# Kernel optimization log

Hardware: AMD Instinct MI355X
Metric: run time of the kernel (lower is better)

The kernel has to match this reference:

```python
import jax, jax.numpy as jnp
import numpy as np

V, F_IN, H, DH, T = 512, 8, 64, 4, 3
E, P, L = 8192, 64, 8
D = H + DH  # path-decoder GRU width


def setup_inputs() -> dict:
    key = jax.random.key(0)
    ks = jax.random.split(key, 24)
    s = 0.1
    inp = {
        "adj_matrix": jax.random.normal(ks[0], (V, V, F_IN), jnp.float32),
        "edges": jax.random.randint(ks[1], (E, 2), 0, V),
        "paths": jax.random.randint(ks[2], (P, L), 0, V),
        "demands": jax.random.uniform(ks[3], (P,), jnp.float32),
        "emb_w": jax.random.normal(ks[4], (H, F_IN), jnp.float32) * s,
        "w1s": jax.random.normal(ks[5], (T, H, H), jnp.float32) * s,
        "w2s": jax.random.normal(ks[6], (T, H, H), jnp.float32) * s,
        "w3s": jax.random.normal(ks[7], (T, H, H), jnp.float32) * s,
        "gru_w_ih": jax.random.normal(ks[8], (3 * H, 2 * H), jnp.float32) * s,
        "gru_w_hh": jax.random.normal(ks[9], (3 * H, H), jnp.float32) * s,
        "gru_b_ih": jax.random.normal(ks[10], (3 * H,), jnp.float32) * s,
        "gru_b_hh": jax.random.normal(ks[11], (3 * H,), jnp.float32) * s,
        "pf_w_ih": jax.random.normal(ks[12], (3 * D, D), jnp.float32) * s,
        "pf_w_hh": jax.random.normal(ks[13], (3 * D, D), jnp.float32) * s,
        "pf_b_ih": jax.random.normal(ks[14], (3 * D,), jnp.float32) * s,
        "pf_b_hh": jax.random.normal(ks[15], (3 * D,), jnp.float32) * s,
        "pb_w_ih": jax.random.normal(ks[16], (3 * D, D), jnp.float32) * s,
        "pb_w_hh": jax.random.normal(ks[17], (3 * D, D), jnp.float32) * s,
        "pb_b_ih": jax.random.normal(ks[18], (3 * D,), jnp.float32) * s,
        "pb_b_hh": jax.random.normal(ks[19], (3 * D,), jnp.float32) * s,
        "wq": jax.random.normal(ks[20], (1, D), jnp.float32) * s,
        "bq": jax.random.normal(ks[21], (1,), jnp.float32) * s,
        "wd": jax.random.normal(ks[22], (DH, 1), jnp.float32) * s,
    }
    return inp


def _gru(x_seq, h0, w_ih, w_hh, b_ih, b_hh):
    """torch-style GRU, batch_first. x_seq (B,Tn,I), h0 (B,Hd) -> (ys, h_last)."""
    def step(h, x_t):
        gi = x_t @ w_ih.T + b_ih
        gh = h @ w_hh.T + b_hh
        ir, iz, inn = jnp.split(gi, 3, axis=-1)
        hr, hz, hn = jnp.split(gh, 3, axis=-1)
        r = jax.nn.sigmoid(ir + hr)
        z = jax.nn.sigmoid(iz + hz)
        n = jnp.tanh(inn + r * hn)
        h_new = (1.0 - z) * n + z * h
        return h_new, h_new
    h_last, ys = jax.lax.scan(step, h0, jnp.swapaxes(x_seq, 0, 1))
    return jnp.swapaxes(ys, 0, 1), h_last


def _message_passing(x, u, v, w1, w2, w3):
    """Vectorized form of the per-edge python loop. x (V,V,Hd), u/v (E,)."""
    Hd = x.shape[-1]
    col_sum = x.sum(axis=0)                      # (V,Hd): sum over first index
    nz_row = jnp.sum(x != 0, axis=-1)            # (V,V) nonzero count per entry
    col_nz = nz_row.sum(axis=0)                  # (V,)
    # incoming edges for edge (u,v): column u, row v zeroed, mean over nonzeros
    s_in = col_sum[u] - x[v, u]                  # (E,Hd)
    n_in = (col_nz[u] - nz_row[v, u]).astype(x.dtype) / Hd
    n_in = jnp.where(n_in == 0, 1.0, n_in)
    e_in = s_in / n_in[:, None]
    # outgoing edges: reversed edge (v,u) -> column v, row u zeroed
    s_out = col_sum[v] - x[u, v]
    n_out = (col_nz[v] - nz_row[u, v]).astype(x.dtype) / Hd
    n_out = jnp.where(n_out == 0, 1.0, n_out)
    e_out = s_out / n_out[:, None]
    m = jax.nn.relu(x[u, v] @ w1.T + e_in @ w2.T + e_out @ w3.T)
    return x.at[u, v].set(m)


def reference(adj_matrix, edges, paths, demands, emb_w, w1s, w2s, w3s,
              gru_w_ih, gru_w_hh, gru_b_ih, gru_b_hh,
              pf_w_ih, pf_w_hh, pf_b_ih, pf_b_hh,
              pb_w_ih, pb_w_hh, pb_b_ih, pb_b_hh, wq, bq, wd):
    u, v = edges[:, 0], edges[:, 1]
    x = adj_matrix @ emb_w.T                     # (V,V,H)
    for t in range(T):
        m = _message_passing(x, u, v, w1s[t], w2s[t], w3s[t])
        inp = jnp.concatenate([m, x], axis=-1)   # (V,V,2H)
        x, _ = _gru(inp, jnp.zeros((x.shape[0], H), x.dtype),
                    gru_w_ih, gru_w_hh, gru_b_ih, gru_b_hh)
    demand_emb = jax.nn.relu(demands[:, None] @ wd.T)        # (P,DH)
    graph_emb = jnp.concatenate([x.mean(axis=(0, 1)),
                                 jnp.zeros((DH,), x.dtype)])  # (D,)
    src, dst = paths[:, :-1], paths[:, 1:]                    # (P,L-1)
    edge_feat = x[src, dst]                                   # (P,L-1,H)
    dem = jnp.broadcast_to(demand_emb[:, None, :], (P, L - 1, DH))
    feat = jnp.concatenate([edge_feat, dem], axis=-1)         # (P,L-1,D)
    h0 = jnp.broadcast_to(graph_emb, (P, D))
    _, hf = _gru(feat, h0, pf_w_ih, pf_w_hh, pf_b_ih, pf_b_hh)
    _, hb = _gru(feat[:, ::-1], h0, pb_w_ih, pb_w_hh, pb_b_ih, pb_b_hh)
    paths_emb = (hf + hb) * 0.5                               # mean over directions
    return jax.nn.softmax(paths_emb @ wq.T + bq, axis=0)      # (P,1)
```

## Files before the change

### kernel.cpp

```cpp
#include <hip/hip_runtime.h>


__device__ __forceinline__ float fsig_(float x) { return 1.f / (1.f + __expf(-x)); }
__device__ __forceinline__ float ftanh_(float x) {
  float e = __expf(2.f * x);
  return 1.f - 2.f / (e + 1.f);
}
__device__ __forceinline__ float sig_(float x) { return 1.f / (1.f + expf(-x)); }

__device__ __forceinline__ void barrier_lgkm() {
  asm volatile("s_waitcnt lgkmcnt(0)\n\ts_barrier" ::: "memory");
}

#define PIN4(v) asm volatile("" : "+v"((v).x), "+v"((v).y), "+v"((v).z), "+v"((v).w))

#define LD4(p) (*(const float4*)(p))
#define DOT4(acc, va, vb)                                                      \
  do {                                                                         \
    acc += (va).x * (vb).x; acc += (va).y * (vb).y;                            \
    acc += (va).z * (vb).z; acc += (va).w * (vb).w;                            \
  } while (0)

#define ALL16(M) M(0) M(1) M(2) M(3) M(4) M(5) M(6) M(7)                       \
                 M(8) M(9) M(10) M(11) M(12) M(13) M(14) M(15)
#define ALLQ(M) M(0,0) M(1,1) M(2,2) M(3,3) M(4,0) M(5,1) M(6,2) M(7,3)        \
                M(8,0) M(9,1) M(10,2) M(11,3) M(12,0) M(13,1) M(14,2) M(15,3)

__global__ __launch_bounds__(256) void embed_kernel(
    const float* __restrict__ adj, const float* __restrict__ emb,
    float* __restrict__ x)
{
  const int64_t row = (int64_t)blockIdx.x * 4 + (threadIdx.x >> 6);
  const int h = threadIdx.x & 63;
  const float* a = adj + row * 8;
  float acc = 0.f;
#pragma unroll
  for (int f = 0; f < 8; ++f) acc += a[f] * emb[h * 8 + f];
  x[row * 64 + h] = acc;
}

__global__ __launch_bounds__(256) void colsum_kernel(
    const float* __restrict__ x, float* __restrict__ col_sum,
    int* __restrict__ col_nz)
{
  const int j = blockIdx.x;
  const int h = threadIdx.x & 63;
  const int w = threadIdx.x >> 6;
  float acc = 0.f;
  int nz = 0;
  for (int i = w; i < 512; i += 4) {
    float v = x[((int64_t)i * 512 + j) * 64 + h];
    acc += v;
    nz += (v != 0.f) ? 1 : 0;
  }
  __shared__ float pacc[4][64];
  __shared__ int pnz[4];
#pragma unroll
  for (int off = 32; off > 0; off >>= 1) nz += __shfl_down(nz, off, 64);
  if (h == 0) pnz[w] = nz;
  pacc[w][h] = acc;
  __syncthreads();
  if (w == 0) {
    col_sum[j * 64 + h] = pacc[0][h] + pacc[1][h] + pacc[2][h] + pacc[3][h];
    if (h == 0) col_nz[j] = pnz[0] + pnz[1] + pnz[2] + pnz[3];
  }
}

__global__ void scatter_idx_kernel(const int* __restrict__ edges,
                                   int* __restrict__ idxmap)
{
  const int e = blockIdx.x * 256 + threadIdx.x;
  if (e < 8192) idxmap[edges[e * 2] * 512 + edges[e * 2 + 1]] = e;
}

__global__ __launch_bounds__(64) void edge_kernel(
    const float* __restrict__ x, const int* __restrict__ edges,
    const float* __restrict__ col_sum, const int* __restrict__ col_nz,
    const float* __restrict__ w1, const float* __restrict__ w2,
    const float* __restrict__ w3, const float* __restrict__ w_ih,
    float* __restrict__ delta_gi)
{
  const int e = blockIdx.x;
  const int h = threadIdx.x;
  const int u = edges[e * 2 + 0];
  const int v = edges[e * 2 + 1];
  __shared__ __align__(16) float xuv[64], ein[64], eout[64], dm[64];
  const float xuvh = x[((int64_t)u * 512 + v) * 64 + h];
  const float xvuh = x[((int64_t)v * 512 + u) * 64 + h];
  xuv[h] = xuvh;
  const int nz_vu = __popcll(__ballot(xvuh != 0.f));
  const int nz_uv = __popcll(__ballot(xuvh != 0.f));
  float n_in = (float)(col_nz[u] - nz_vu) / 64.f;
  if (n_in == 0.f) n_in = 1.f;
  float n_out = (float)(col_nz[v] - nz_uv) / 64.f;
  if (n_out == 0.f) n_out = 1.f;
  ein[h] = (col_sum[u * 64 + h] - xvuh) / n_in;
  eout[h] = (col_sum[v * 64 + h] - xuvh) / n_out;
  __syncthreads();
  const float4* w1r = (const float4*)(w1 + h * 64);
  const float4* w2r = (const float4*)(w2 + h * 64);
  const float4* w3r = (const float4*)(w3 + h * 64);
  const float4* xuv4 = (const float4*)xuv;
  const float4* ein4 = (const float4*)ein;
  const float4* eout4 = (const float4*)eout;
  float acc = 0.f;
#pragma unroll
  for (int kk = 0; kk < 16; ++kk) {
    float4 a = xuv4[kk], b = w1r[kk];
    acc += a.x * b.x + a.y * b.y + a.z * b.z + a.w * b.w;
    a = ein4[kk]; b = w2r[kk];
    acc += a.x * b.x + a.y * b.y + a.z * b.z + a.w * b.w;
    a = eout4[kk]; b = w3r[kk];
    acc += a.x * b.x + a.y * b.y + a.z * b.z + a.w * b.w;
  }
  const float m = fmaxf(acc, 0.f);
  dm[h] = m - xuvh;
  __syncthreads();
  const float4* dm4 = (const float4*)dm;
#pragma unroll
  for (int r = 0; r < 3; ++r) {
    const int gg = h + r * 64;
    const float4* wr = (const float4*)(w_ih + gg * 128);
    float d = 0.f;
#pragma unroll
    for (int kk = 0; kk < 16; ++kk) {
      float4 a = dm4[kk], b = wr[kk];
      d += a.x * b.x + a.y * b.y + a.z * b.z + a.w * b.w;
    }
    delta_gi[e * 192 + gg] = d;
  }
}

#define DECL_W(i)                                                              \
  float4 W##i; {                                                               \
    float4 t0 = LD4(wg + 4 * (i));                                             \
    float4 t1 = LD4(wg + 64 + 4 * (i));                                        \
    W##i.x = t0.x + t1.x; W##i.y = t0.y + t1.y;                                \
    W##i.z = t0.z + t1.z; W##i.w = t0.w + t1.w;                                \
  }                                                                            \
  PIN4(W##i);
#define DECL_X(i) float4 X##i = LD4(xrow + 4 * (i));
#define PQ(i, q) { DOT4(ac##q, X##i, W##i); X##i = LD4(xnext + 4 * (i)); }
#define DECL_WR(i) float4 WR##i = LD4(wr_ + 4 * (i)); PIN4(WR##i);
#define DECL_WZ(i) float4 WZ##i = LD4(wz_ + 4 * (i)); PIN4(WZ##i);
#define DECL_WN(i) float4 WN##i = LD4(wn_ + 4 * (i)); PIN4(WN##i);
#define CCHUNK(i)                                                              \
  { float4 hc = hs4[(i)];                                                      \
    DOT4(racc, hc, WR##i); DOT4(zacc, hc, WZ##i); DOT4(nacc, hc, WN##i); }

__global__ __launch_bounds__(256, 2) void scan_kernel(
    float* __restrict__ x, const float* __restrict__ delta_gi,
    const int* __restrict__ idxmap,
    const float* __restrict__ w_ih, const float* __restrict__ w_hh,
    const float* __restrict__ b_ih, const float* __restrict__ b_hh)
{
  const int b = blockIdx.x;
  const int tid = threadIdx.x;
  __shared__ __align__(16) float hs[64];
  __shared__ float gib[2][192];
  __shared__ int idxl[512];
  float* xrow = x + (int64_t)b * 32768;

  for (int i = tid; i < 512; i += 256) idxl[i] = idxmap[b * 512 + i];

  if (tid < 192) {
    const int g = tid;
    const float* wg = w_ih + g * 128;
    ALL16(DECL_W)
    const float bi = b_ih[g];
    ALL16(DECL_X)
    __syncthreads();
    {
      float ac0 = bi, ac1 = 0.f, ac2 = 0.f, ac3 = 0.f;
      const float* xnext = xrow + 64;
      ALLQ(PQ)
      float acc = (ac0 + ac1) + (ac2 + ac3);
      const int i0 = idxl[0];
      if (i0 >= 0) acc += delta_gi[(int64_t)i0 * 192 + g];
      gib[0][g] = acc;
    }
    const int idx1 = idxl[1];
    float dgn = 0.f;
    if (idx1 >= 0) dgn = delta_gi[(int64_t)idx1 * 192 + g];
    barrier_lgkm();
    for (int t = 0; t < 512; ++t) {
      if (t < 511) {
        const int tn2 = (t + 2 < 512) ? (t + 2) : 511;
        const float* xnext = xrow + tn2 * 64;
        float ac0 = bi + dgn, ac1 = 0.f, ac2 = 0.f, ac3 = 0.f;
        ALLQ(PQ)
        gib[(t + 1) & 1][g] = (ac0 + ac1) + (ac2 + ac3);
        const int idxn = idxl[tn2];
        dgn = 0.f;
        if (idxn >= 0) dgn = delta_gi[(int64_t)idxn * 192 + g];
      }
      barrier_lgkm();
    }
  } else {
    const int j = tid - 192;
    const float* wr_ = w_hh + j * 64;
    const float* wz_ = w_hh + (j + 64) * 64;
    const float* wn_ = w_hh + (j + 128) * 64;
    ALL16(DECL_WR)
    ALL16(DECL_WZ)
    ALL16(DECL_WN)
    const float bhr = b_hh[j], bhz = b_hh[j + 64], bhn = b_hh[j + 128];
    float hj = 0.f;
    hs[j] = 0.f;
    __syncthreads();
    __builtin_amdgcn_s_setprio(1);
    barrier_lgkm();
    const float4* hs4 = (const float4*)hs;
    for (int t = 0; t < 512; ++t) {
      const float gr = gib[t & 1][j];
      const float gz = gib[t & 1][64 + j];
      const float gn = gib[t & 1][128 + j];
      float racc = bhr, zacc = bhz, nacc = bhn;
      ALL16(CCHUNK)
      const float r = fsig_(gr + racc);
      const float z = fsig_(gz + zacc);
      const float n = ftanh_(gn + r * nacc);
      hj = (1.f - z) * n + z * hj;
      hs[j] = hj;
      xrow[t * 64 + j] = hj;
      barrier_lgkm();
    }
  }
}

__global__ __launch_bounds__(64) void graphemb_kernel(
    const float* __restrict__ col_sum, float* __restrict__ graph_emb)
{
  const int h = threadIdx.x;
  float s = 0.f;
#pragma unroll 8
  for (int j = 0; j < 512; ++j) s += col_sum[j * 64 + h];
  graph_emb[h] = s * (1.f / 262144.f);
  if (h < 4) graph_emb[64 + h] = 0.f;
}

__global__ __launch_bounds__(256) void path_kernel(
    const float* __restrict__ x, const int* __restrict__ paths,
    const float* __restrict__ demands, const float* __restrict__ wd,
    const float* __restrict__ graph_emb,
    const float* __restrict__ wih_f, const float* __restrict__ whh_f,
    const float* __restrict__ bih_f, const float* __restrict__ bhh_f,
    const float* __restrict__ wih_b, const float* __restrict__ whh_b,
    const float* __restrict__ bih_b, const float* __restrict__ bhh_b,
    float* __restrict__ h_out)
{
  const int p = blockIdx.x & 63;
  const int dir = blockIdx.x >> 6;
  const int g = threadIdx.x;
  const float* w_ih = dir ? wih_b : wih_f;
  const float* w_hh = dir ? whh_b : whh_f;
  const float* bih = dir ? bih_b : bih_f;
  const float* bhh = dir ? bhh_b : bhh_f;
  __shared__ float feat[7][68], hs[68], rbuf[68], zbuf[68];
  if (g < 68) {
#pragma unroll
    for (int t = 0; t < 7; ++t) {
      const int src = paths[p * 8 + t];
      const int dst = paths[p * 8 + t + 1];
      feat[t][g] = (g < 64) ? x[((int64_t)src * 512 + dst) * 64 + g]
                            : fmaxf(demands[p] * wd[g - 64], 0.f);
    }
    hs[g] = graph_emb[g];
  }
  __syncthreads();
  for (int s = 0; s < 7; ++s) {
    const int t = dir ? (6 - s) : s;
    float acc = 0.f, hacc = 0.f;
    if (g < 204) {
      acc = bih[g];
      hacc = bhh[g];
      for (int k = 0; k < 68; ++k) {
        acc += feat[t][k] * w_ih[g * 68 + k];
        hacc += hs[k] * w_hh[g * 68 + k];
      }
    }
    if (g < 68) rbuf[g] = sig_(acc + hacc);
    else if (g < 136) zbuf[g - 68] = sig_(acc + hacc);
    __syncthreads();
    if (g >= 136 && g < 204) {
      const int j = g - 136;
      const float n = tanhf(acc + rbuf[j] * hacc);
      const float z = zbuf[j];
      const float hn = (1.f - z) * n + z * hs[j];
      hs[j] = hn;
    }
    __syncthreads();
  }
  if (g < 68) h_out[(dir * 64 + p) * 68 + g] = hs[g];
}

__global__ __launch_bounds__(64) void combine_kernel(
    const float* __restrict__ h_out, const float* __restrict__ wq,
    const float* __restrict__ bq, float* __restrict__ out)
{
  const int p = threadIdx.x;
  float l = bq[0];
#pragma unroll
  for (int d = 0; d < 68; ++d)
    l += 0.5f * (h_out[p * 68 + d] + h_out[(64 + p) * 68 + d]) * wq[d];
  float mx = l;
#pragma unroll
  for (int off = 32; off > 0; off >>= 1) mx = fmaxf(mx, __shfl_xor(mx, off, 64));
  const float e = expf(l - mx);
  float s = e;
#pragma unroll
  for (int off = 32; off > 0; off >>= 1) s += __shfl_xor(s, off, 64);
  out[p] = e / s;
}

extern "C" void kernel_launch(void* const* d_in, const int* in_sizes, int n_in,
                              void* d_out, int out_size, void* d_ws, size_t ws_size,
                              hipStream_t stream)
{
  const float* adj = (const float*)d_in[0];
  const int* edges = (const int*)d_in[1];
  const int* paths = (const int*)d_in[2];
  const float* demands = (const float*)d_in[3];
  const float* emb_w = (const float*)d_in[4];
  const float* w1s = (const float*)d_in[5];
  const float* w2s = (const float*)d_in[6];
  const float* w3s = (const float*)d_in[7];
  const float* gru_w_ih = (const float*)d_in[8];
  const float* gru_w_hh = (const float*)d_in[9];
  const float* gru_b_ih = (const float*)d_in[10];
  const float* gru_b_hh = (const float*)d_in[11];
  const float* pf_w_ih = (const float*)d_in[12];
  const float* pf_w_hh = (const float*)d_in[13];
  const float* pf_b_ih = (const float*)d_in[14];
  const float* pf_b_hh = (const float*)d_in[15];
  const float* pb_w_ih = (const float*)d_in[16];
  const float* pb_w_hh = (const float*)d_in[17];
  const float* pb_b_ih = (const float*)d_in[18];
  const float* pb_b_hh = (const float*)d_in[19];
  const float* wq = (const float*)d_in[20];
  const float* bq = (const float*)d_in[21];
  const float* wd = (const float*)d_in[22];
  float* out = (float*)d_out;

  float* xA = (float*)d_ws;
  float* col_sum = xA + 16777216;
  int* col_nz = (int*)(col_sum + 32768);
  int* idxmap = col_nz + 512;
  float* delta_gi = (float*)(idxmap + 262144);
  float* graph_emb = delta_gi + 1572864;
  float* h_out = graph_emb + 128;

  hipMemsetAsync(idxmap, 0xFF, 262144 * sizeof(int), stream);
  scatter_idx_kernel<<<32, 256, 0, stream>>>(edges, idxmap);
  embed_kernel<<<65536, 256, 0, stream>>>(adj, emb_w, xA);

  for (int t = 0; t < 3; ++t) {
    colsum_kernel<<<512, 256, 0, stream>>>(xA, col_sum, col_nz);
    edge_kernel<<<8192, 64, 0, stream>>>(xA, edges, col_sum, col_nz,
        w1s + t * 4096, w2s + t * 4096, w3s + t * 4096, gru_w_ih, delta_gi);
    scan_kernel<<<512, 256, 0, stream>>>(xA, delta_gi, idxmap,
        gru_w_ih, gru_w_hh, gru_b_ih, gru_b_hh);
  }

  colsum_kernel<<<512, 256, 0, stream>>>(xA, col_sum, col_nz);
  graphemb_kernel<<<1, 64, 0, stream>>>(col_sum, graph_emb);
  path_kernel<<<128, 256, 0, stream>>>(xA, paths, demands, wd, graph_emb,
      pf_w_ih, pf_w_hh, pf_b_ih, pf_b_hh,
      pb_w_ih, pb_w_hh, pb_b_ih, pb_b_hh, h_out);
  combine_kernel<<<1, 64, 0, stream>>>(h_out, wq, bq, out);
}
```

Measured before the change: 1.863 ms.

## Split GRU hidden recurrence across three waves and prefetch x rows into LDS ring

The scan kernel grows from 256 to 384 threads. The old single recurrent wave computed the r, z and n gates together. Now two waves compute r and z each and write them to LDS, while a third wave computes n and updates h. This shortens the serial per-step dependency chain at the cost of an extra barrier per timestep. The input-projection waves now read x rows from a 16-entry LDS ring, which wave 0 fills asynchronously via global_load_lds eight steps ahead, replacing per-thread global loads in the loop.

Measured after the change: 1.980 ms. +6.3%, slower.

```diff
diff --git a/kernel.cpp b/kernel.cpp
--- a/kernel.cpp
+++ b/kernel.cpp
@@ -13,6 +13,11 @@
 }
 
 #define PIN4(v) asm volatile("" : "+v"((v).x), "+v"((v).y), "+v"((v).z), "+v"((v).w))
+
+#define GLD_LDS4(gp, lp)                                                       \
+  __builtin_amdgcn_global_load_lds(                                            \
+      (const __attribute__((address_space(1))) void*)(gp),                     \
+      (__attribute__((address_space(3))) void*)(lp), 4, 0, 0)
 
 #define LD4(p) (*(const float4*)(p))
 #define DOT4(acc, va, vb)                                                      \
@@ -139,88 +144,108 @@
     W##i.z = t0.z + t1.z; W##i.w = t0.w + t1.w;                                \
   }                                                                            \
   PIN4(W##i);
-#define DECL_X(i) float4 X##i = LD4(xrow + 4 * (i));
-#define PQ(i, q) { DOT4(ac##q, X##i, W##i); X##i = LD4(xnext + 4 * (i)); }
-#define DECL_WR(i) float4 WR##i = LD4(wr_ + 4 * (i)); PIN4(WR##i);
-#define DECL_WZ(i) float4 WZ##i = LD4(wz_ + 4 * (i)); PIN4(WZ##i);
-#define DECL_WN(i) float4 WN##i = LD4(wn_ + 4 * (i)); PIN4(WN##i);
-#define CCHUNK(i)                                                              \
-  { float4 hc = hs4[(i)];                                                      \
-    DOT4(racc, hc, WR##i); DOT4(zacc, hc, WZ##i); DOT4(nacc, hc, WN##i); }
-
-__global__ __launch_bounds__(256, 2) void scan_kernel(
+#define PX(i, q) { float4 xc = xq4[(i)]; DOT4(a##q, xc, W##i); }
+#define DECL_WC(i) float4 WC##i = LD4(wc + 4 * (i)); PIN4(WC##i);
+#define HQ(i, q) { float4 hc = hs4[(i)]; DOT4(a##q, hc, WC##i); }
+
+__global__ __launch_bounds__(384, 2) void scan_kernel(
     float* __restrict__ x, const float* __restrict__ delta_gi,
     const int* __restrict__ idxmap,
     const float* __restrict__ w_ih, const float* __restrict__ w_hh,
     const float* __restrict__ b_ih, const float* __restrict__ b_hh)
 {
+  const int tid = threadIdx.x;
+  const int wave = tid >> 6;
+  const int lane = tid & 63;
   const int b = blockIdx.x;
-  const int tid = threadIdx.x;
+  __shared__ __align__(16) float xring[16][64];
+  __shared__ float gib[2][192];
+  __shared__ float rzb[2][64];
   __shared__ __align__(16) float hs[64];
-  __shared__ float gib[2][192];
   __shared__ int idxl[512];
   float* xrow = x + (int64_t)b * 32768;
 
-  for (int i = tid; i < 512; i += 256) idxl[i] = idxmap[b * 512 + i];
-
-  if (tid < 192) {
-    const int g = tid;
+  for (int i = tid; i < 512; i += 384) idxl[i] = idxmap[b * 512 + i];
+  if (tid < 64) hs[tid] = 0.f;
+  if (wave == 0) {
+#pragma unroll
+    for (int s = 0; s < 8; ++s) GLD_LDS4(xrow + s * 64 + lane, &xring[s][0]);
+  }
+  __syncthreads();
+
+  if (wave < 3) {
+    const int g = wave * 64 + lane;
     const float* wg = w_ih + g * 128;
     ALL16(DECL_W)
     const float bi = b_ih[g];
-    ALL16(DECL_X)
-    __syncthreads();
     {
-      float ac0 = bi, ac1 = 0.f, ac2 = 0.f, ac3 = 0.f;
-      const float* xnext = xrow + 64;
-      ALLQ(PQ)
-      float acc = (ac0 + ac1) + (ac2 + ac3);
+      const float4* xq4 = (const float4*)&xring[0][0];
+      float a0 = bi, a1 = 0.f, a2 = 0.f, a3 = 0.f;
+      ALLQ(PX)
+      float acc = (a0 + a1) + (a2 + a3);
       const int i0 = idxl[0];
-      if (i0 >= 0) acc += delta_gi[(int64_t)i0 * 192 + g];
+      const float d0 = delta_gi[(int64_t)(i0 < 0 ? 0 : i0) * 192 + g];
+      acc += (i0 >= 0) ? d0 : 0.f;
       gib[0][g] = acc;
     }
-    const int idx1 = idxl[1];
-    float dgn = 0.f;
-    if (idx1 >= 0) dgn = delta_gi[(int64_t)idx1 * 192 + g];
+    const int i1 = idxl[1];
+    float dg_cur = delta_gi[(int64_t)(i1 < 0 ? 0 : i1) * 192 + g];
+    dg_cur = (i1 >= 0) ? dg_cur : 0.f;
     barrier_lgkm();
     for (int t = 0; t < 512; ++t) {
-      if (t < 511) {
-        const int tn2 = (t + 2 < 512) ? (t + 2) : 511;
-        const float* xnext = xrow + tn2 * 64;
-        float ac0 = bi + dgn, ac1 = 0.f, ac2 = 0.f, ac3 = 0.f;
-        ALLQ(PQ)
-        gib[(t + 1) & 1][g] = (ac0 + ac1) + (ac2 + ac3);
-        const int idxn = idxl[tn2];
-        dgn = 0.f;
-        if (idxn >= 0) dgn = delta_gi[(int64_t)idxn * 192 + g];
+      const float4* xq4 = (const float4*)&xring[(t + 1) & 15][0];
+      float a0 = bi + dg_cur, a1 = 0.f, a2 = 0.f, a3 = 0.f;
+      ALLQ(PX)
+      gib[(t + 1) & 1][g] = (a0 + a1) + (a2 + a3);
+      const int t2 = (t + 2 < 512) ? t + 2 : 511;
+      const int idn = idxl[t2];
+      float dgt = delta_gi[(int64_t)(idn < 0 ? 0 : idn) * 192 + g];
+      dgt = (idn >= 0) ? dgt : 0.f;
+      if (wave == 0) {
+        const int tf = (t + 8 < 512) ? t + 8 : 511;
+        GLD_LDS4(xrow + tf * 64 + lane, &xring[(t + 8) & 15][0]);
+        asm volatile("s_waitcnt vmcnt(6)" ::: "memory");
       }
       barrier_lgkm();
-    }
-  } else {
-    const int j = tid - 192;
-    const float* wr_ = w_hh + j * 64;
-    const float* wz_ = w_hh + (j + 64) * 64;
-    const float* wn_ = w_hh + (j + 128) * 64;
-    ALL16(DECL_WR)
-    ALL16(DECL_WZ)
-    ALL16(DECL_WN)
-    const float bhr = b_hh[j], bhz = b_hh[j + 64], bhn = b_hh[j + 128];
-    float hj = 0.f;
-    hs[j] = 0.f;
-    __syncthreads();
+      barrier_lgkm();
+      dg_cur = dgt;
+    }
+  } else if (wave < 5) {
+    const int cls = wave - 3;
+    const int j = lane;
+    const float* wc = w_hh + (cls * 64 + j) * 64;
+    ALL16(DECL_WC)
+    const float bc = b_hh[cls * 64 + j];
     __builtin_amdgcn_s_setprio(1);
     barrier_lgkm();
     const float4* hs4 = (const float4*)hs;
     for (int t = 0; t < 512; ++t) {
-      const float gr = gib[t & 1][j];
-      const float gz = gib[t & 1][64 + j];
+      const float gc = gib[t & 1][cls * 64 + j];
+      float a0 = bc, a1 = 0.f, a2 = 0.f, a3 = 0.f;
+      ALLQ(HQ)
+      rzb[cls][j] = fsig_(gc + (a0 + a1) + (a2 + a3));
+      barrier_lgkm();
+      barrier_lgkm();
+    }
+  } else {
+    const int j = lane;
+    const float* wc = w_hh + (128 + j) * 64;
+    ALL16(DECL_WC)
+    const float bc = b_hh[128 + j];
+    float hj = 0.f;
+    __builtin_amdgcn_s_setprio(1);
+    barrier_lgkm();
+    const float4* hs4 = (const float4*)hs;
+    for (int t = 0; t < 512; ++t) {
       const float gn = gib[t & 1][128 + j];
-      float racc = bhr, zacc = bhz, nacc = bhn;
-      ALL16(CCHUNK)
-      const float r = fsig_(gr + racc);
-      const float z = fsig_(gz + zacc);
-      const float n = ftanh_(gn + r * nacc);
-      hj = (1.f - z) * n + z * hj;
+      float a0 = bc, a1 = 0.f, a2 = 0.f, a3 = 0.f;
+      ALLQ(HQ)
+      const float nacc = (a0 + a1) + (a2 + a3);
+      barrier_lgkm();
+      const float r = rzb[0][j];
+      const float z = rzb[1][j];
+      const float nn = ftanh_(gn + r * nacc);
+      hj = (1.f - z) * nn + z * hj;
       hs[j] = hj;
       xrow[t * 64 + j] = hj;
       barrier_lgkm();
@@ -358,7 +383,7 @@
     colsum_kernel<<<512, 256, 0, stream>>>(xA, col_sum, col_nz);
     edge_kernel<<<8192, 64, 0, stream>>>(xA, edges, col_sum, col_nz,
         w1s + t * 4096, w2s + t * 4096, w3s + t * 4096, gru_w_ih, delta_gi);
-    scan_kernel<<<512, 256, 0, stream>>>(xA, delta_gi, idxmap,
+    scan_kernel<<<512, 384, 0, stream>>>(xA, delta_gi, idxmap,
         gru_w_ih, gru_w_hh, gru_b_ih, gru_b_hh);
   }
 
```
